# Performance work log

Hardware: AMD Instinct MI355X
Metric: run time of the kernel (lower is better)

The kernel has to match this reference:

```python
import jax, jax.numpy as jnp
import numpy as np

TAU = 1.0   # temperature
BETA = 1.0  # instance_alingment_weight


def setup_inputs() -> dict:
    key = jax.random.key(0)
    k1, k2, k3 = jax.random.split(key, 3)
    N, D = 1024, 128
    return {
        "x": jax.random.normal(k1, (N, D), dtype=jnp.float32),
        "aug_x": jax.random.normal(k2, (N, D), dtype=jnp.float32),
        "label_prompt_embedding": jax.random.normal(k3, (N, D), dtype=jnp.float32),
    }


def _pair_loss(x, y, scale):
    # positive distances: ||x_i - y_i|| / (tau * sqrt(D)), shape [N]
    pos = jnp.linalg.norm(x - y, axis=1) * scale
    # pairwise distance matrix [N, N] via broadcasted [N, N, D] diff (as original)
    dm = jnp.linalg.norm(x[:, None, :] - y[None, :, :], axis=-1) * scale
    denom = jnp.sum(jnp.exp(dm), axis=1)  # [N]
    # log(exp(pos) / denom) == pos - log(denom)
    return jnp.mean(pos - jnp.log(denom))


def reference(x, aug_x, label_prompt_embedding):
    D = x.shape[-1]
    scale = 1.0 / (TAU * np.sqrt(D).astype(np.float32))
    center_alignment_loss = _pair_loss(x, label_prompt_embedding, scale)
    instance_alignment_loss = _pair_loss(x, aug_x, scale)
    alignment_loss = center_alignment_loss + BETA * instance_alignment_loss
    return (alignment_loss, center_alignment_loss, instance_alignment_loss)
```

## Files before the change

### kernel.cpp

```cpp
#include <hip/hip_runtime.h>
#include <math.h>

#define NN 1024
#define DD 128

typedef __bf16 bf16x8 __attribute__((ext_vector_type(8)));
typedef float  floatx4 __attribute__((ext_vector_type(4)));

__global__ __launch_bounds__(1024) void align_fused(
    const float* __restrict__ x, const float* __restrict__ lp,
    const float* __restrict__ aug, float* __restrict__ out)
{
    const float SCALE = 0.08838834764831845f;
    const int p    = blockIdx.y;
    const float* __restrict__ Y = p ? aug : lp;
    const int i0   = blockIdx.x * 16;
    const int tid  = threadIdx.x;
    const int w    = tid >> 6;
    const int lane = tid & 63;
    const int col  = lane & 15;
    const int quad = lane >> 4;

    const float* xrow = x + (size_t)(i0 + col) * DD + quad * 8;
    bf16x8 afrag[4];
    float nx_own = 0.f;
#pragma unroll
    for (int c = 0; c < 4; ++c) {
        const float4 u0 = *(const float4*)(xrow + c * 32);
        const float4 u1 = *(const float4*)(xrow + c * 32 + 4);
        nx_own += u0.x*u0.x + u0.y*u0.y + u0.z*u0.z + u0.w*u0.w;
        nx_own += u1.x*u1.x + u1.y*u1.y + u1.z*u1.z + u1.w*u1.w;
        bf16x8 f;
        f[0]=(__bf16)u0.x; f[1]=(__bf16)u0.y; f[2]=(__bf16)u0.z; f[3]=(__bf16)u0.w;
        f[4]=(__bf16)u1.x; f[5]=(__bf16)u1.y; f[6]=(__bf16)u1.z; f[7]=(__bf16)u1.w;
        afrag[c] = f;
    }
    nx_own += __shfl_xor(nx_own, 16);
    nx_own += __shfl_xor(nx_own, 32);
    float nxr[4];
#pragma unroll
    for (int r = 0; r < 4; ++r) nxr[r] = __shfl(nx_own, quad * 4 + r);

    float denom[4] = {0.f, 0.f, 0.f, 0.f};
    float pos[4]   = {0.f, 0.f, 0.f, 0.f};

#pragma unroll
    for (int t = 0; t < 4; ++t) {
        const int j0 = w * 64 + t * 16;
        const float* yrow = Y + (size_t)(j0 + col) * DD + quad * 8;
        bf16x8 bfrag[4];
        float ny_own = 0.f;
#pragma unroll
        for (int c = 0; c < 4; ++c) {
            const float4 u0 = *(const float4*)(yrow + c * 32);
            const float4 u1 = *(const float4*)(yrow + c * 32 + 4);
            ny_own += u0.x*u0.x + u0.y*u0.y + u0.z*u0.z + u0.w*u0.w;
            ny_own += u1.x*u1.x + u1.y*u1.y + u1.z*u1.z + u1.w*u1.w;
            bf16x8 f;
            f[0]=(__bf16)u0.x; f[1]=(__bf16)u0.y; f[2]=(__bf16)u0.z; f[3]=(__bf16)u0.w;
            f[4]=(__bf16)u1.x; f[5]=(__bf16)u1.y; f[6]=(__bf16)u1.z; f[7]=(__bf16)u1.w;
            bfrag[c] = f;
        }
        ny_own += __shfl_xor(ny_own, 16);
        ny_own += __shfl_xor(ny_own, 32);

        floatx4 acc = {0.f, 0.f, 0.f, 0.f};
#pragma unroll
        for (int c = 0; c < 4; ++c)
            acc = __builtin_amdgcn_mfma_f32_16x16x32_bf16(afrag[c], bfrag[c], acc, 0, 0, 0);

#pragma unroll
        for (int r = 0; r < 4; ++r) {
            const int row = quad * 4 + r;
            float d2 = fmaf(-2.f, acc[r], nxr[r] + ny_own);
            d2 = fmaxf(d2, 0.f);
            const float dm = SCALE * sqrtf(d2);
            denom[r] += __expf(dm);
            if (j0 + col == i0 + row) pos[r] = dm;
        }
    }

#pragma unroll
    for (int r = 0; r < 4; ++r) {
#pragma unroll
        for (int m = 1; m < 16; m <<= 1) {
            denom[r] += __shfl_xor(denom[r], m);
            pos[r]   += __shfl_xor(pos[r], m);
        }
    }

    __shared__ float ld_den[16][16];
    __shared__ float ld_pos[16][16];
    if (col == 0) {
#pragma unroll
        for (int r = 0; r < 4; ++r) {
            ld_den[w][quad * 4 + r] = denom[r];
            ld_pos[w][quad * 4 + r] = pos[r];
        }
    }
    __syncthreads();
    float s = 0.f;
    if (tid < 16) {
        float den = 0.f, po = 0.f;
#pragma unroll
        for (int ww = 0; ww < 16; ++ww) {
            den += ld_den[ww][tid];
            po  += ld_pos[ww][tid];
        }
        s = po - logf(den);
#pragma unroll
        for (int m = 1; m < 16; m <<= 1) s += __shfl_xor(s, m);
    }
    if (tid == 0) {
        const float v = s * (1.0f / (float)NN);
        unsigned* uo = (unsigned*)out;
        atomicCAS(&uo[0], 0xAAAAAAAAu, 0u);
        atomicCAS(&uo[1], 0xAAAAAAAAu, 0u);
        atomicCAS(&uo[2], 0xAAAAAAAAu, 0u);
        atomicAdd(&out[0], v);
        atomicAdd(&out[1 + p], v);
    }
}

extern "C" void kernel_launch(void* const* d_in, const int* in_sizes, int n_in,
                              void* d_out, int out_size, void* d_ws, size_t ws_size,
                              hipStream_t stream) {
    const float* x   = (const float*)d_in[0];
    const float* aug = (const float*)d_in[1];
    const float* lp  = (const float*)d_in[2];
    float* out       = (float*)d_out;
    align_fused<<<dim3(64, 2), 1024, 0, stream>>>(x, lp, aug, out);
}
```

Baseline: 82.17 us.

## Split column range across blocks and add separate finalize kernel

The fused kernel now runs on a 64x2x8 grid of 256-thread blocks, each handling one 128-column chunk of the distance matrix instead of all 1024 columns. Partial denominators and positive distances go to a workspace buffer. A second single-block kernel sums them, takes logs and writes the three outputs directly, with no atomics. This spreads the work over many more CUs, at the cost of an extra kernel launch and redundant reloads of the X rows in each chunk.

```diff
diff --git a/kernel.cpp b/kernel.cpp
--- a/kernel.cpp
+++ b/kernel.cpp
@@ -7,14 +7,19 @@
 typedef __bf16 bf16x8 __attribute__((ext_vector_type(8)));
 typedef float  floatx4 __attribute__((ext_vector_type(4)));
 
-__global__ __launch_bounds__(1024) void align_fused(
+__global__ __launch_bounds__(256) void align_main(
     const float* __restrict__ x, const float* __restrict__ lp,
-    const float* __restrict__ aug, float* __restrict__ out)
+    const float* __restrict__ aug,
+    float* __restrict__ denom_part ,
+    float* __restrict__ posbuf     )
 {
     const float SCALE = 0.08838834764831845f;
-    const int p    = blockIdx.y;
+    const int bx = blockIdx.x;
+    const int p  = blockIdx.y;
+    const int jc = blockIdx.z;
     const float* __restrict__ Y = p ? aug : lp;
-    const int i0   = blockIdx.x * 16;
+
+    const int i0   = bx * 16;
     const int tid  = threadIdx.x;
     const int w    = tid >> 6;
     const int lane = tid & 63;
@@ -45,8 +50,8 @@
     float pos[4]   = {0.f, 0.f, 0.f, 0.f};
 
 #pragma unroll
-    for (int t = 0; t < 4; ++t) {
-        const int j0 = w * 64 + t * 16;
+    for (int t = 0; t < 2; ++t) {
+        const int j0 = jc * 128 + t * 64 + w * 16;
         const float* yrow = Y + (size_t)(j0 + col) * DD + quad * 8;
         bf16x8 bfrag[4];
         float ny_own = 0.f;
@@ -89,8 +94,8 @@
         }
     }
 
-    __shared__ float ld_den[16][16];
-    __shared__ float ld_pos[16][16];
+    __shared__ float ld_den[4][16];
+    __shared__ float ld_pos[4][16];
     if (col == 0) {
 #pragma unroll
         for (int r = 0; r < 4; ++r) {
@@ -99,26 +104,52 @@
         }
     }
     __syncthreads();
-    float s = 0.f;
     if (tid < 16) {
-        float den = 0.f, po = 0.f;
+        const float den = ld_den[0][tid] + ld_den[1][tid] + ld_den[2][tid] + ld_den[3][tid];
+        denom_part[(size_t)(p * 8 + jc) * NN + i0 + tid] = den;
+        if (jc == (bx >> 3)) {
+            const float po = ld_pos[0][tid] + ld_pos[1][tid] + ld_pos[2][tid] + ld_pos[3][tid];
+            posbuf[p * NN + i0 + tid] = po;
+        }
+    }
+}
+
+__global__ __launch_bounds__(256) void align_fin(
+    const float* __restrict__ denom_part, const float* __restrict__ posbuf,
+    float* __restrict__ out)
+{
+    const int tid  = threadIdx.x;
+    const int w    = tid >> 6;
+    const int lane = tid & 63;
+    float sum0 = 0.f, sum1 = 0.f;
 #pragma unroll
-        for (int ww = 0; ww < 16; ++ww) {
-            den += ld_den[ww][tid];
-            po  += ld_pos[ww][tid];
+    for (int k = 0; k < 4; ++k) {
+        const int row = tid + k * 256;
+#pragma unroll
+        for (int p = 0; p < 2; ++p) {
+            float den = 0.f;
+#pragma unroll
+            for (int jc = 0; jc < 8; ++jc)
+                den += denom_part[(size_t)(p * 8 + jc) * NN + row];
+            const float c = posbuf[p * NN + row] - __logf(den);
+            if (p) sum1 += c; else sum0 += c;
         }
-        s = po - logf(den);
+    }
 #pragma unroll
-        for (int m = 1; m < 16; m <<= 1) s += __shfl_xor(s, m);
+    for (int m = 1; m < 64; m <<= 1) {
+        sum0 += __shfl_xor(sum0, m);
+        sum1 += __shfl_xor(sum1, m);
     }
+    __shared__ float s0[4], s1[4];
+    if (lane == 0) { s0[w] = sum0; s1[w] = sum1; }
+    __syncthreads();
     if (tid == 0) {
-        const float v = s * (1.0f / (float)NN);
-        unsigned* uo = (unsigned*)out;
-        atomicCAS(&uo[0], 0xAAAAAAAAu, 0u);
-        atomicCAS(&uo[1], 0xAAAAAAAAu, 0u);
-        atomicCAS(&uo[2], 0xAAAAAAAAu, 0u);
-        atomicAdd(&out[0], v);
-        atomicAdd(&out[1 + p], v);
+        const float inv = 1.0f / (float)NN;
+        const float c  = (s0[0] + s0[1] + s0[2] + s0[3]) * inv;
+        const float ia = (s1[0] + s1[1] + s1[2] + s1[3]) * inv;
+        out[0] = c + ia;
+        out[1] = c;
+        out[2] = ia;
     }
 }
 
@@ -129,5 +160,10 @@
     const float* aug = (const float*)d_in[1];
     const float* lp  = (const float*)d_in[2];
     float* out       = (float*)d_out;
-    align_fused<<<dim3(64, 2), 1024, 0, stream>>>(x, lp, aug, out);
+
+    float* denom_part = (float*)d_ws;
+    float* posbuf     = (float*)((char*)d_ws + 65536);
+
+    align_main<<<dim3(64, 2, 8), 256, 0, stream>>>(x, lp, aug, denom_part, posbuf);
+    align_fin<<<1, 256, 0, stream>>>(denom_part, posbuf, out);
 }
```

New measurement: 72.20 us. 1.14x faster.
